# Performance work log

Measured on AMD Instinct MI355X. Metric: run time of the kernel, lower is better.

## Reference

```python
import jax, jax.numpy as jnp
import numpy as np
from jax import lax

B, DIM, H, W = 2, 64, 512, 512
HEADS, NKEYS, MDIM = 8, 4, 4
CH = DIM // HEADS  # per-head channels = 8
EPS = 1e-12  # F.normalize eps


def conv2d(x, w, b, pad, groups=1):
    # x: NCHW, w: OIHW
    y = lax.conv_general_dilated(
        x, w, window_strides=(1, 1), padding=[(pad, pad), (pad, pad)],
        feature_group_count=groups,
        dimension_numbers=("NCHW", "OIHW", "NCHW"))
    return y + b[None, :, None, None]


def setup_inputs() -> dict:
    ks = jax.random.split(jax.random.key(0), 12)
    x = jax.random.normal(ks[0], (B, DIM, H, W), dtype=jnp.float32)
    metainfo = jax.random.normal(ks[1], (B, NKEYS, MDIM), dtype=jnp.float32)
    # per-meta-key Linear(meta_dims, dim), stacked: [n, dim, meta_dims]
    Wq = jax.random.normal(ks[2], (NKEYS, DIM, MDIM), dtype=jnp.float32) / np.sqrt(MDIM)
    bq = jax.random.normal(ks[3], (NKEYS, DIM), dtype=jnp.float32) * 0.01
    temps = jnp.ones((NKEYS, HEADS), dtype=jnp.float32)  # init ones, shape (heads,1,1) per key
    kv_w = jax.random.normal(ks[4], (2 * DIM, DIM, 1, 1), dtype=jnp.float32) / np.sqrt(DIM)
    kv_b = jax.random.normal(ks[5], (2 * DIM,), dtype=jnp.float32) * 0.01
    dw_w = jax.random.normal(ks[6], (2 * DIM, 1, 3, 3), dtype=jnp.float32) / 3.0
    dw_b = jax.random.normal(ks[7], (2 * DIM,), dtype=jnp.float32) * 0.01
    cc1_w = jax.random.normal(ks[8], (DIM, 1, 3, 3), dtype=jnp.float32) / 3.0
    cc1_b = jax.random.normal(ks[9], (DIM,), dtype=jnp.float32) * 0.01
    cc2_w = jax.random.normal(ks[10], (DIM, DIM, 1, 1), dtype=jnp.float32) / np.sqrt(DIM)
    cc2_b = jax.random.normal(ks[11], (DIM,), dtype=jnp.float32) * 0.01
    return {"x": x, "metainfo": metainfo, "Wq": Wq, "bq": bq, "temps": temps,
            "kv_w": kv_w, "kv_b": kv_b, "dw_w": dw_w, "dw_b": dw_b,
            "cc1_w": cc1_w, "cc1_b": cc1_b, "cc2_w": cc2_w, "cc2_b": cc2_b}


def reference(x, metainfo, Wq, bq, temps, kv_w, kv_b, dw_w, dw_b,
              cc1_w, cc1_b, cc2_w, cc2_b):
    b, c, h, w = x.shape
    ch = c // HEADS
    # per-key linear projection of metadata -> queries [b, n, heads, ch]
    q = jnp.einsum("bnd,nkd->bnk", metainfo, Wq) + bq[None]
    q = q.reshape(b, NKEYS, HEADS, ch)
    # F.normalize over the singleton query-length dim -> elementwise sign scaling
    q = q / jnp.maximum(jnp.abs(q), EPS)
    # kv: 1x1 conv then 3x3 depthwise conv
    kv = conv2d(x, kv_w, kv_b, pad=0)
    kv = conv2d(kv, dw_w, dw_b, pad=1, groups=2 * c)
    k, v = jnp.split(kv, 2, axis=1)
    k = k.reshape(b, HEADS, ch, h * w)
    k = k / jnp.maximum(jnp.linalg.norm(k, axis=-1, keepdims=True), EPS)
    v = v.reshape(b, HEADS, ch, h * w)
    # attention: [b, n, heads, hw] (query length is 1 per meta key)
    attn = jnp.einsum("bnec,becs->bnes", q, k) * temps[None, :, :, None]
    attn = jax.nn.softmax(attn, axis=-1)
    # broadcast matmul over spatial grid + sum over meta keys, fused:
    # out[b,c,s] = sum_n sum_head attn[b,n,head,s] * v[b,head,c,s]
    out = jnp.einsum("bnes,becs->bcs", attn, v).reshape(b, ch, h, w)
    # cross_conv: grouped 3x3 (ch -> dim, groups=ch), GELU, 1x1
    out = conv2d(out, cc1_w, cc1_b, pad=1, groups=ch)
    out = jax.nn.gelu(out, approximate=False)
    out = conv2d(out, cc2_w, cc2_b, pad=0)
    return out
```

## Files before the change

kernel.cpp:

```cpp
#include <hip/hip_runtime.h>
#include <hip/hip_bf16.h>

#define B_    2
#define H_    512
#define W_    512
#define HW_   262144
#define EPSV  1e-12f

typedef __hip_bfloat16 bf16;
typedef __fp16 h16x8 __attribute__((ext_vector_type(8)));
typedef float f32x4 __attribute__((ext_vector_type(4)));

__global__ __launch_bounds__(256) void k1a_conv1x1(
    const float* __restrict__ x, const float* __restrict__ kv_w,
    const float* __restrict__ kv_b, bf16* __restrict__ kv1) {
  const int tid = threadIdx.x;
  const int p0 = blockIdx.x * 128;
  const int b  = p0 >> 18;
  const int s0 = p0 & (HW_ - 1);
  __shared__ __fp16 Wl[8 * 128 * 8];
  __shared__ __fp16 Xe[8 * 64 * 8];
  __shared__ __fp16 Xo[8 * 64 * 8];

  {
    const int o = tid >> 1, half = tid & 1;
    const float* wp = kv_w + o * 64 + half * 32;
#pragma unroll
    for (int j = 0; j < 4; ++j) {
      const float4 a = *reinterpret_cast<const float4*>(wp + j * 8);
      const float4 c = *reinterpret_cast<const float4*>(wp + j * 8 + 4);
      h16x8 h;
      h[0] = (__fp16)a.x; h[1] = (__fp16)a.y; h[2] = (__fp16)a.z; h[3] = (__fp16)a.w;
      h[4] = (__fp16)c.x; h[5] = (__fp16)c.y; h[6] = (__fp16)c.z; h[7] = (__fp16)c.w;
      *reinterpret_cast<h16x8*>(&Wl[((half * 4 + j) * 128 + o) * 8]) = h;
    }
  }
  {
    const int m = tid & 63, kgq = tid >> 6;
    const float* xp = x + (size_t)b * 64 * HW_ + s0 + m * 2;
#pragma unroll
    for (int kk = 0; kk < 2; ++kk) {
      const int kg = kgq * 2 + kk;
      h16x8 he, ho;
#pragma unroll
      for (int e = 0; e < 8; ++e) {
        const float2 v =
            *reinterpret_cast<const float2*>(xp + (size_t)(kg * 8 + e) * HW_);
        he[e] = (__fp16)v.x; ho[e] = (__fp16)v.y;
      }
      *reinterpret_cast<h16x8*>(&Xe[(kg * 64 + m) * 8]) = he;
      *reinterpret_cast<h16x8*>(&Xo[(kg * 64 + m) * 8]) = ho;
    }
  }
  __syncthreads();

  const int wv = tid >> 6, lane = tid & 63;
  const int m0 = (wv & 1) * 64, n0 = (wv >> 1) * 64;
  const int lr = lane & 15, lg = lane >> 4;
  const __fp16* xb2 = (lr & 1) ? Xo : Xe;
  f32x4 acc[4][4];
#pragma unroll
  for (int mt = 0; mt < 4; ++mt)
#pragma unroll
    for (int nt = 0; nt < 4; ++nt) acc[mt][nt] = (f32x4){0.f, 0.f, 0.f, 0.f};
#pragma unroll
  for (int ks = 0; ks < 2; ++ks) {
    h16x8 af[4], bfr[4];
#pragma unroll
    for (int mt = 0; mt < 4; ++mt)
      af[mt] = *reinterpret_cast<const h16x8*>(
          &Wl[((ks * 4 + lg) * 128 + m0 + mt * 16 + lr) * 8]);
#pragma unroll
    for (int nt = 0; nt < 4; ++nt)
      bfr[nt] = *reinterpret_cast<const h16x8*>(
          &xb2[((ks * 4 + lg) * 64 + (n0 >> 1) + nt * 8 + (lr >> 1)) * 8]);
#pragma unroll
    for (int mt = 0; mt < 4; ++mt)
#pragma unroll
      for (int nt = 0; nt < 4; ++nt)
        acc[mt][nt] = __builtin_amdgcn_mfma_f32_16x16x32_f16(
            af[mt], bfr[nt], acc[mt][nt], 0, 0, 0);
  }
  bf16* dst = kv1 + (size_t)b * 128 * HW_ + s0;
#pragma unroll
  for (int mt = 0; mt < 4; ++mt) {
#pragma unroll
    for (int r = 0; r < 4; ++r) {
      const int o = m0 + mt * 16 + lg * 4 + r;
      const float bv = kv_b[o];
      bf16* op = dst + (size_t)o * HW_;
#pragma unroll
      for (int nt = 0; nt < 4; ++nt)
        op[n0 + nt * 16 + lr] = __float2bfloat16(acc[mt][nt][r] + bv);
    }
  }
}

__global__ __launch_bounds__(256) void k1b_dw(
    const bf16* __restrict__ kv1, const float* __restrict__ dw_w,
    const float* __restrict__ dw_b, bf16* __restrict__ kvout,
    float* __restrict__ ssqpart) {
  const int tid = threadIdx.x;
  const int cchunk = tid & 63;
  const int ch_sub = tid >> 6;
  const int rs = blockIdx.x;
  const int chgrp = blockIdx.y;
  const int b = blockIdx.z;
  const int ch = chgrp * 4 + ch_sub;
  const int c0 = cchunk * 8;
  const int r0 = rs * 32;
  const bf16* src = kv1 + (size_t)(b * 128 + ch) * HW_;
  const bool is_k = (ch < 64);
  const size_t obase = is_k ? (size_t)(b * 64 + ch) * HW_
                            : (size_t)(128 + b * 64 + (ch - 64)) * HW_;
  bf16* dst = kvout + obase;
  float dwr[9];
#pragma unroll
  for (int t = 0; t < 9; ++t) dwr[t] = dw_w[ch * 9 + t];
  const float bd = dw_b[ch];

  float a0[10], a1[10], a2[10];
  auto loadrow = [&](int gr, float* a) {
    if (gr < 0 || gr >= H_) {
#pragma unroll
      for (int t = 0; t < 10; ++t) a[t] = 0.f;
      return;
    }
    union { int4 v; bf16 h[8]; } raw;
    raw.v = *reinterpret_cast<const int4*>(src + (size_t)gr * W_ + c0);
#pragma unroll
    for (int t = 0; t < 8; ++t) a[t + 1] = __bfloat162float(raw.h[t]);
    const float left = __shfl_up(a[8], 1);
    const float right = __shfl_down(a[1], 1);
    a[0] = (cchunk == 0) ? 0.f : left;
    a[9] = (cchunk == 63) ? 0.f : right;
  };
  loadrow(r0 - 1, a0);
  loadrow(r0, a1);
  float sq = 0.f;
#pragma unroll 4
  for (int rr = 0; rr < 32; ++rr) {
    loadrow(r0 + rr + 1, a2);
    union { int4 v; bf16 h[8]; } ou;
#pragma unroll
    for (int j = 0; j < 8; ++j) {
      const float ov = bd
          + dwr[0] * a0[j] + dwr[1] * a0[j + 1] + dwr[2] * a0[j + 2]
          + dwr[3] * a1[j] + dwr[4] * a1[j + 1] + dwr[5] * a1[j + 2]
          + dwr[6] * a2[j] + dwr[7] * a2[j + 1] + dwr[8] * a2[j + 2];
      sq += ov * ov;
      ou.h[j] = __float2bfloat16(ov);
    }
    *reinterpret_cast<int4*>(dst + (size_t)(r0 + rr) * W_ + c0) = ou.v;
#pragma unroll
    for (int t = 0; t < 10; ++t) { a0[t] = a1[t]; a1[t] = a2[t]; }
  }
#pragma unroll
  for (int off = 32; off > 0; off >>= 1) sq += __shfl_down(sq, off, 64);
  if (is_k && cchunk == 0)
    ssqpart[(size_t)(b * 64 + ch) * 16 + rs] = sq;
}

__global__ __launch_bounds__(256) void k2_finalize(
    const float* __restrict__ ssqpart, const float* __restrict__ temps,
    const float* __restrict__ metainfo, const float* __restrict__ Wq,
    const float* __restrict__ bq, float* __restrict__ rnorm,
    float* __restrict__ qn) {
  const int tid = threadIdx.x;
  if (tid < 128) {
    const int b = tid >> 6, c = tid & 63;
    float s = 0.f;
    for (int p = 0; p < 16; ++p) s += ssqpart[(size_t)(b * 64 + c) * 16 + p];
    rnorm[tid] = 1.f / fmaxf(sqrtf(s), EPSV);
  }
  __syncthreads();
  for (int idx = tid; idx < 512; idx += 256) {
    const int b = idx >> 8, n = (idx >> 6) & 3, d = idx & 63;
    float acc = bq[n * 64 + d];
#pragma unroll
    for (int m = 0; m < 4; ++m)
      acc += metainfo[(b * 4 + n) * 4 + m] * Wq[(n * 64 + d) * 4 + m];
    const float sgn = acc / fmaxf(fabsf(acc), EPSV);
    qn[idx] = sgn * rnorm[b * 64 + d] * temps[n * 8 + (d >> 3)];
  }
}

__global__ __launch_bounds__(256) void k3_denom(
    const bf16* __restrict__ kbuf, const float* __restrict__ qn,
    float* __restrict__ dpart) {
  const int tile = blockIdx.x, e = blockIdx.y, b = blockIdx.z;
  const int tid = threadIdx.x;
  float q[4][8];
#pragma unroll
  for (int n = 0; n < 4; ++n)
#pragma unroll
    for (int cc = 0; cc < 8; ++cc)
      q[n][cc] = qn[b * 256 + n * 64 + e * 8 + cc];
  const bf16* kb = kbuf + (size_t)(b * 64 + e * 8) * HW_;
  float dsum[4] = {0.f, 0.f, 0.f, 0.f};
  const int sbase = tile * 4096;
#pragma unroll
  for (int it = 0; it < 2; ++it) {
    const int s = sbase + (it * 256 + tid) * 8;
    float kf[8][8];
#pragma unroll
    for (int cc = 0; cc < 8; ++cc) {
      union { int4 v; bf16 h[8]; } r;
      r.v = *reinterpret_cast<const int4*>(kb + (size_t)cc * HW_ + s);
#pragma unroll
      for (int j = 0; j < 8; ++j) kf[cc][j] = __bfloat162float(r.h[j]);
    }
#pragma unroll
    for (int n = 0; n < 4; ++n) {
#pragma unroll
      for (int px = 0; px < 8; ++px) {
        float l = 0.f;
#pragma unroll
        for (int cc = 0; cc < 8; ++cc) l += q[n][cc] * kf[cc][px];
        dsum[n] += __expf(l);
      }
    }
  }
  __shared__ float red[256];
#pragma unroll
  for (int n = 0; n < 4; ++n) {
    red[tid] = dsum[n];
    __syncthreads();
    for (int st = 128; st > 0; st >>= 1) {
      if (tid < st) red[tid] += red[tid + st];
      __syncthreads();
    }
    if (tid == 0) dpart[(b * 32 + n * 8 + e) * 64 + tile] = red[0];
    __syncthreads();
  }
}

__global__ __launch_bounds__(256) void k4_attend(
    const bf16* __restrict__ kvbuf, const float* __restrict__ qn,
    const float* __restrict__ dpart, float* __restrict__ mid) {
  const int b = blockIdx.y;
  const int tid = threadIdx.x;
  __shared__ float qnl[256];
  __shared__ float rdl[32];
  qnl[tid] = qn[b * 256 + tid];
  if (tid < 32) {
    float s = 0.f;
    for (int t = 0; t < 64; ++t) s += dpart[(b * 32 + tid) * 64 + t];
    rdl[tid] = 1.f / s;
  }
  __syncthreads();
  const bf16* kb = kvbuf + (size_t)(b * 64) * HW_;
  const bf16* vb = kvbuf + (size_t)(128 + b * 64) * HW_;
  float* mb = mid + (size_t)b * 8 * HW_;
  const int s = (blockIdx.x * 256 + tid) * 4;
  float macc[8][4];
#pragma unroll
  for (int cc = 0; cc < 8; ++cc)
#pragma unroll
    for (int px = 0; px < 4; ++px) macc[cc][px] = 0.f;
#pragma unroll
  for (int e = 0; e < 8; ++e) {
    float kf[8][4];
#pragma unroll
    for (int cc = 0; cc < 8; ++cc) {
      union { ushort4 v; bf16 h[4]; } r;
      r.v = *reinterpret_cast<const ushort4*>(kb + (size_t)(e * 8 + cc) * HW_ + s);
#pragma unroll
      for (int px = 0; px < 4; ++px) kf[cc][px] = __bfloat162float(r.h[px]);
    }
    float wsum[4] = {0.f, 0.f, 0.f, 0.f};
#pragma unroll
    for (int n = 0; n < 4; ++n) {
      const float rd = rdl[n * 8 + e];
#pragma unroll
      for (int px = 0; px < 4; ++px) {
        float l = 0.f;
#pragma unroll
        for (int cc = 0; cc < 8; ++cc) l += qnl[n * 64 + e * 8 + cc] * kf[cc][px];
        wsum[px] += __expf(l) * rd;
      }
    }
#pragma unroll
    for (int cc = 0; cc < 8; ++cc) {
      union { ushort4 v; bf16 h[4]; } r;
      r.v = *reinterpret_cast<const ushort4*>(vb + (size_t)(e * 8 + cc) * HW_ + s);
#pragma unroll
      for (int px = 0; px < 4; ++px)
        macc[cc][px] += wsum[px] * __bfloat162float(r.h[px]);
    }
  }
#pragma unroll
  for (int cc = 0; cc < 8; ++cc)
    *reinterpret_cast<float4*>(mb + (size_t)cc * HW_ + s) =
        make_float4(macc[cc][0], macc[cc][1], macc[cc][2], macc[cc][3]);
}

__global__ __launch_bounds__(256) void k5_cross(
    const float* __restrict__ mid, const float* __restrict__ cc1_w,
    const float* __restrict__ cc1_b, const float* __restrict__ cc2_w,
    const float* __restrict__ cc2_b, float* __restrict__ out) {
  const int tid = threadIdx.x;
  const int c0 = blockIdx.x * 128;
  const int r0 = blockIdx.y * 2;
  const int b = blockIdx.z;
  __shared__ float midl[8 * 4 * 132];
  __shared__ __fp16 gs[256 * 64];
  __shared__ __fp16 w2s[64 * 64];
  __shared__ float w1l[576];
  __shared__ float b1l[64], b2l[64];
  for (int idx = tid; idx < 8 * 4 * 130; idx += 256) {
    const int ch = idx / 520;
    const int rem = idx % 520;
    const int dr = rem / 130, lc = rem % 130;
    const int gr = r0 - 1 + dr, gc = c0 - 1 + lc;
    float v = 0.f;
    if (gr >= 0 && gr < H_ && gc >= 0 && gc < W_)
      v = mid[(size_t)(b * 8 + ch) * HW_ + (size_t)gr * W_ + gc];
    midl[(ch * 4 + dr) * 132 + lc] = v;
  }
#pragma unroll
  for (int rr = 0; rr < 2; ++rr) {
    const int idx = tid + rr * 256;
    const int p = idx >> 3, ooc = idx & 7;
    const float4 a = *reinterpret_cast<const float4*>(cc2_w + p * 64 + ooc * 8);
    const float4 c = *reinterpret_cast<const float4*>(cc2_w + p * 64 + ooc * 8 + 4);
    h16x8 h;
    h[0] = (__fp16)a.x; h[1] = (__fp16)a.y; h[2] = (__fp16)a.z; h[3] = (__fp16)a.w;
    h[4] = (__fp16)c.x; h[5] = (__fp16)c.y; h[6] = (__fp16)c.z; h[7] = (__fp16)c.w;
    *reinterpret_cast<h16x8*>(&w2s[p * 64 + ((ooc ^ (p & 7)) << 3)]) = h;
  }
  for (int idx = tid; idx < 576; idx += 256) w1l[idx] = cc1_w[idx];
  if (tid < 64) { b1l[tid] = cc1_b[tid]; b2l[tid] = cc2_b[tid]; }
  __syncthreads();

  {
    const int ty = tid >> 5, tx = tid & 31;
    const int rl = tx >> 4;
    const int cb = (tx & 15) * 8;
    float m[3][10];
#pragma unroll
    for (int dr = 0; dr < 3; ++dr)
#pragma unroll
      for (int t = 0; t < 10; ++t)
        m[dr][t] = midl[(ty * 4 + rl + dr) * 132 + cb + t];
    const int pxb = rl * 128 + cb;
#pragma unroll
    for (int hh = 0; hh < 2; ++hh) {
      float g[8][4];
#pragma unroll
      for (int j = 0; j < 8; ++j) {
        const int oo = ty * 8 + j;
        float w[9];
#pragma unroll
        for (int t = 0; t < 9; ++t) w[t] = w1l[oo * 9 + t];
        const float bb = b1l[oo];
#pragma unroll
        for (int i2 = 0; i2 < 4; ++i2) {
          const int i = hh * 4 + i2;
          float a = bb;
#pragma unroll
          for (int dr = 0; dr < 3; ++dr)
#pragma unroll
            for (int dc = 0; dc < 3; ++dc)
              a += w[dr * 3 + dc] * m[dr][i + dc];
          g[j][i2] = 0.5f * a * (1.f + erff(a * 0.70710678118654752f));
        }
      }
#pragma unroll
      for (int i2 = 0; i2 < 4; ++i2) {
        const int px = pxb + hh * 4 + i2;
        const int swz = (px ^ (px >> 3)) & 7;
        h16x8 h;
#pragma unroll
        for (int j = 0; j < 8; ++j) h[j] = (__fp16)g[j][i2];
        *reinterpret_cast<h16x8*>(&gs[px * 64 + ((ty ^ swz) << 3)]) = h;
      }
    }
  }
  __syncthreads();

  const int wv = tid >> 6, lane = tid & 63;
  const int n0 = wv * 64;
  const int lr = lane & 15, lg = lane >> 4;
  f32x4 acc[4][4];
#pragma unroll
  for (int mt = 0; mt < 4; ++mt)
#pragma unroll
    for (int nt = 0; nt < 4; ++nt) acc[mt][nt] = (f32x4){0.f, 0.f, 0.f, 0.f};
#pragma unroll
  for (int ks = 0; ks < 2; ++ks) {
    const int ooc = ks * 4 + lg;
    h16x8 af[4], bfr[4];
#pragma unroll
    for (int mt = 0; mt < 4; ++mt) {
      const int p = mt * 16 + lr;
      af[mt] = *reinterpret_cast<const h16x8*>(
          &w2s[p * 64 + ((ooc ^ (p & 7)) << 3)]);
    }
#pragma unroll
    for (int nt = 0; nt < 4; ++nt) {
      const int px = n0 + nt * 16 + lr;
      const int swz = (px ^ (px >> 3)) & 7;
      bfr[nt] = *reinterpret_cast<const h16x8*>(
          &gs[px * 64 + ((ooc ^ swz) << 3)]);
    }
#pragma unroll
    for (int mt = 0; mt < 4; ++mt)
#pragma unroll
      for (int nt = 0; nt < 4; ++nt)
        acc[mt][nt] = __builtin_amdgcn_mfma_f32_16x16x32_f16(
            af[mt], bfr[nt], acc[mt][nt], 0, 0, 0);
  }
#pragma unroll
  for (int mt = 0; mt < 4; ++mt) {
#pragma unroll
    for (int r = 0; r < 4; ++r) {
      const int p = mt * 16 + lg * 4 + r;
      const float bv = b2l[p];
      float* op = out + (size_t)(b * 64 + p) * HW_;
#pragma unroll
      for (int nt = 0; nt < 4; ++nt) {
        const int px = n0 + nt * 16 + lr;
        const int grow = r0 + (px >> 7), gcol = c0 + (px & 127);
        op[(size_t)grow * W_ + gcol] = acc[mt][nt][r] + bv;
      }
    }
  }
}

extern "C" void kernel_launch(void* const* d_in, const int* in_sizes, int n_in,
                              void* d_out, int out_size, void* d_ws, size_t ws_size,
                              hipStream_t stream) {
  const float* x        = (const float*)d_in[0];
  const float* metainfo = (const float*)d_in[1];
  const float* Wq       = (const float*)d_in[2];
  const float* bq       = (const float*)d_in[3];
  const float* temps    = (const float*)d_in[4];
  const float* kv_w     = (const float*)d_in[5];
  const float* kv_b     = (const float*)d_in[6];
  const float* dw_w     = (const float*)d_in[7];
  const float* dw_b     = (const float*)d_in[8];
  const float* cc1_w    = (const float*)d_in[9];
  const float* cc1_b    = (const float*)d_in[10];
  const float* cc2_w    = (const float*)d_in[11];
  const float* cc2_b    = (const float*)d_in[12];
  float* out = (float*)d_out;

  float* ws      = (float*)d_ws;
  bf16*  kv1     = (bf16*)d_ws;
  float* mid     = ws + 33554432;
  float* small_  = ws + 37748736;
  float* ssqpart = small_;
  float* rnorm   = small_ + 2560;
  float* qn      = small_ + 2688;
  float* dpart   = small_ + 3200;

  bf16* kvout = (bf16*)d_out;

  k1a_conv1x1<<<4096, 256, 0, stream>>>(x, kv_w, kv_b, kv1);
  k1b_dw<<<dim3(16, 32, 2), 256, 0, stream>>>(kv1, dw_w, dw_b, kvout, ssqpart);
  k2_finalize<<<1, 256, 0, stream>>>(ssqpart, temps, metainfo, Wq, bq,
                                     rnorm, qn);
  k3_denom<<<dim3(64, 8, 2), 256, 0, stream>>>(kvout, qn, dpart);
  k4_attend<<<dim3(256, 2), 256, 0, stream>>>(kvout, qn, dpart, mid);
  k5_cross<<<dim3(4, 256, 2), 256, 0, stream>>>(mid, cc1_w, cc1_b, cc2_w,
                                                cc2_b, out);
}
```

Measured before the change: 297.8 us.

## Make conv1x1 blocks persistent over four tiles with register-prefetched double buffering

```diff
diff --git a/kernel.cpp b/kernel.cpp
--- a/kernel.cpp
+++ b/kernel.cpp
@@ -15,12 +15,12 @@
     const float* __restrict__ x, const float* __restrict__ kv_w,
     const float* __restrict__ kv_b, bf16* __restrict__ kv1) {
   const int tid = threadIdx.x;
-  const int p0 = blockIdx.x * 128;
-  const int b  = p0 >> 18;
-  const int s0 = p0 & (HW_ - 1);
+  const int base = blockIdx.x * 512;
+  const int b  = base >> 18;
+  const int sb = base & (HW_ - 1);
   __shared__ __fp16 Wl[8 * 128 * 8];
-  __shared__ __fp16 Xe[8 * 64 * 8];
-  __shared__ __fp16 Xo[8 * 64 * 8];
+  __shared__ __fp16 Xe[2][8 * 64 * 8];
+  __shared__ __fp16 Xo[2][8 * 64 * 8];
 
   {
     const int o = tid >> 1, half = tid & 1;
@@ -35,63 +35,79 @@
       *reinterpret_cast<h16x8*>(&Wl[((half * 4 + j) * 128 + o) * 8]) = h;
     }
   }
-  {
-    const int m = tid & 63, kgq = tid >> 6;
-    const float* xp = x + (size_t)b * 64 * HW_ + s0 + m * 2;
-#pragma unroll
-    for (int kk = 0; kk < 2; ++kk) {
-      const int kg = kgq * 2 + kk;
-      h16x8 he, ho;
-#pragma unroll
-      for (int e = 0; e < 8; ++e) {
-        const float2 v =
-            *reinterpret_cast<const float2*>(xp + (size_t)(kg * 8 + e) * HW_);
-        he[e] = (__fp16)v.x; ho[e] = (__fp16)v.y;
-      }
-      *reinterpret_cast<h16x8*>(&Xe[(kg * 64 + m) * 8]) = he;
-      *reinterpret_cast<h16x8*>(&Xo[(kg * 64 + m) * 8]) = ho;
-    }
-  }
-  __syncthreads();
+  const int m = tid & 63, kgq = tid >> 6;
+  const float* xbase = x + (size_t)b * 64 * HW_ + sb + m * 2;
+
+  float2 cur[16], nxt[16];
+#pragma unroll
+  for (int u = 0; u < 16; ++u)
+    cur[u] = *reinterpret_cast<const float2*>(xbase + (size_t)(kgq * 16 + u) * HW_);
 
   const int wv = tid >> 6, lane = tid & 63;
   const int m0 = (wv & 1) * 64, n0 = (wv >> 1) * 64;
   const int lr = lane & 15, lg = lane >> 4;
-  const __fp16* xb2 = (lr & 1) ? Xo : Xe;
-  f32x4 acc[4][4];
-#pragma unroll
-  for (int mt = 0; mt < 4; ++mt)
-#pragma unroll
-    for (int nt = 0; nt < 4; ++nt) acc[mt][nt] = (f32x4){0.f, 0.f, 0.f, 0.f};
-#pragma unroll
-  for (int ks = 0; ks < 2; ++ks) {
-    h16x8 af[4], bfr[4];
+
+#pragma unroll
+  for (int t = 0; t < 4; ++t) {
+    if (t < 3) {
+#pragma unroll
+      for (int u = 0; u < 16; ++u)
+        nxt[u] = *reinterpret_cast<const float2*>(
+            xbase + (t + 1) * 128 + (size_t)(kgq * 16 + u) * HW_);
+    }
+#pragma unroll
+    for (int kk = 0; kk < 2; ++kk) {
+      h16x8 he, ho;
+#pragma unroll
+      for (int e = 0; e < 8; ++e) {
+        he[e] = (__fp16)cur[kk * 8 + e].x;
+        ho[e] = (__fp16)cur[kk * 8 + e].y;
+      }
+      const int kg = kgq * 2 + kk;
+      *reinterpret_cast<h16x8*>(&Xe[t & 1][(kg * 64 + m) * 8]) = he;
+      *reinterpret_cast<h16x8*>(&Xo[t & 1][(kg * 64 + m) * 8]) = ho;
+    }
+    __syncthreads();
+    const __fp16* xb2 = (lr & 1) ? Xo[t & 1] : Xe[t & 1];
+    f32x4 acc[4][4];
 #pragma unroll
     for (int mt = 0; mt < 4; ++mt)
-      af[mt] = *reinterpret_cast<const h16x8*>(
-          &Wl[((ks * 4 + lg) * 128 + m0 + mt * 16 + lr) * 8]);
-#pragma unroll
-    for (int nt = 0; nt < 4; ++nt)
-      bfr[nt] = *reinterpret_cast<const h16x8*>(
-          &xb2[((ks * 4 + lg) * 64 + (n0 >> 1) + nt * 8 + (lr >> 1)) * 8]);
-#pragma unroll
-    for (int mt = 0; mt < 4; ++mt)
+#pragma unroll
+      for (int nt = 0; nt < 4; ++nt) acc[mt][nt] = (f32x4){0.f, 0.f, 0.f, 0.f};
+#pragma unroll
+    for (int ks = 0; ks < 2; ++ks) {
+      h16x8 af[4], bfr[4];
+#pragma unroll
+      for (int mt = 0; mt < 4; ++mt)
+        af[mt] = *reinterpret_cast<const h16x8*>(
+            &Wl[((ks * 4 + lg) * 128 + m0 + mt * 16 + lr) * 8]);
 #pragma unroll
       for (int nt = 0; nt < 4; ++nt)
-        acc[mt][nt] = __builtin_amdgcn_mfma_f32_16x16x32_f16(
-            af[mt], bfr[nt], acc[mt][nt], 0, 0, 0);
-  }
-  bf16* dst = kv1 + (size_t)b * 128 * HW_ + s0;
-#pragma unroll
-  for (int mt = 0; mt < 4; ++mt) {
-#pragma unroll
-    for (int r = 0; r < 4; ++r) {
-      const int o = m0 + mt * 16 + lg * 4 + r;
-      const float bv = kv_b[o];
-      bf16* op = dst + (size_t)o * HW_;
-#pragma unroll
-      for (int nt = 0; nt < 4; ++nt)
-        op[n0 + nt * 16 + lr] = __float2bfloat16(acc[mt][nt][r] + bv);
+        bfr[nt] = *reinterpret_cast<const h16x8*>(
+            &xb2[((ks * 4 + lg) * 64 + (n0 >> 1) + nt * 8 + (lr >> 1)) * 8]);
+#pragma unroll
+      for (int mt = 0; mt < 4; ++mt)
+#pragma unroll
+        for (int nt = 0; nt < 4; ++nt)
+          acc[mt][nt] = __builtin_amdgcn_mfma_f32_16x16x32_f16(
+              af[mt], bfr[nt], acc[mt][nt], 0, 0, 0);
+    }
+    bf16* dst = kv1 + (size_t)b * 128 * HW_ + sb + t * 128;
+#pragma unroll
+    for (int mt = 0; mt < 4; ++mt) {
+#pragma unroll
+      for (int r = 0; r < 4; ++r) {
+        const int o = m0 + mt * 16 + lg * 4 + r;
+        const float bv = kv_b[o];
+        bf16* op = dst + (size_t)o * HW_;
+#pragma unroll
+        for (int nt = 0; nt < 4; ++nt)
+          op[n0 + nt * 16 + lr] = __float2bfloat16(acc[mt][nt][r] + bv);
+      }
+    }
+    if (t < 3) {
+#pragma unroll
+      for (int u = 0; u < 16; ++u) cur[u] = nxt[u];
     }
   }
 }
@@ -457,7 +473,7 @@
 
   bf16* kvout = (bf16*)d_out;
 
-  k1a_conv1x1<<<4096, 256, 0, stream>>>(x, kv_w, kv_b, kv1);
+  k1a_conv1x1<<<1024, 256, 0, stream>>>(x, kv_w, kv_b, kv1);
   k1b_dw<<<dim3(16, 32, 2), 256, 0, stream>>>(kv1, dw_w, dw_b, kvout, ssqpart);
   k2_finalize<<<1, 256, 0, stream>>>(ssqpart, temps, metainfo, Wq, bq,
                                      rnorm, qn);
```

Measured after the change: 278.3 us. -6.6%, faster.
